# Performance work log

Hardware: AMD Instinct MI355X
Metric: run time of the kernel (lower is better)

The kernel has to match this reference:

```python
import jax, jax.numpy as jnp
import numpy as np

B, N, C = 4, 4096, 128

def setup_inputs() -> dict:
    key = jax.random.key(0)
    ks = jax.random.split(key, 7)
    s = 1.0 / np.sqrt(C)
    return {
        "x": jax.random.normal(ks[0], (B, N, C), dtype=jnp.float32),
        "Wq": jax.random.uniform(ks[1], (C, C), jnp.float32, -s, s),
        "bq": jax.random.uniform(ks[2], (C,), jnp.float32, -s, s),
        "Wk": jax.random.uniform(ks[3], (C, C), jnp.float32, -s, s),
        "bk": jax.random.uniform(ks[4], (C,), jnp.float32, -s, s),
        "Wv": jax.random.uniform(ks[5], (C, C), jnp.float32, -s, s),
        "bv": jax.random.uniform(ks[6], (C,), jnp.float32, -s, s),
    }

def reference(x, Wq, bq, Wk, bk, Wv, bv):
    # GELU-activated Q/K/V projections (torch default GELU = exact erf form)
    q = jax.nn.gelu(jnp.einsum("bnc,dc->bnd", x, Wq) + bq, approximate=False)
    k = jax.nn.gelu(jnp.einsum("bnc,dc->bnd", x, Wk) + bk, approximate=False)
    v = jax.nn.gelu(jnp.einsum("bnc,dc->bnd", x, Wv) + bv, approximate=False)
    # Unscaled attention: softmax(Q K^T) V
    scores = jnp.einsum("bnd,bmd->bnm", q, k)  # [B, N, N]
    attn = jax.nn.softmax(scores, axis=-1)
    return jnp.einsum("bnm,bmd->bnd", attn, v)
```

## Files before the change

### kernel.cpp

```cpp
#include <hip/hip_runtime.h>
#include <hip/hip_bf16.h>
#include <math.h>

#define BATCH 4
#define SEQ   4096
#define CDIM  128
#define NROWS (BATCH * SEQ)
#define KVB   32
#define NTILE (SEQ / KVB)
#define KTILE_B 8192
#define VTILE_B 8192
#define STAGE_B (KTILE_B + VTILE_B)
#define LOG2E 1.4426950408889634f

typedef __attribute__((ext_vector_type(4))) float    f32x4;
typedef __attribute__((ext_vector_type(8))) _Float16 half8;
typedef __attribute__((ext_vector_type(4))) short    bf16x4;
typedef __attribute__((ext_vector_type(8))) short    bf16x8;

__device__ __forceinline__ float bf2f(short s) {
  unsigned u = ((unsigned)(unsigned short)s) << 16;
  return __builtin_bit_cast(float, u);
}
__device__ __forceinline__ short f2bf(float f) {
  __hip_bfloat16 h = __float2bfloat16(f);
  return __builtin_bit_cast(short, h);
}
__device__ __forceinline__ float gelu_exact(float v) {
  return 0.5f * v * (1.0f + erff(v * 0.70710678118654752440f));
}
__device__ __forceinline__ int kswz_h(int r, int c) {
  int slot  = c >> 3;
  int slotp = (slot & 8) | ((slot ^ r) & 7);
  return r * 128 + slotp * 8 + (c & 7);
}
__device__ __forceinline__ void gl_lds16(const void* g, void* l) {
  __builtin_amdgcn_global_load_lds(
      (const __attribute__((address_space(1))) void*)g,
      (__attribute__((address_space(3))) void*)l, 16, 0, 0);
}

__global__ void wprep_kernel(const float* __restrict__ Wq,
                             const float* __restrict__ Wk,
                             const float* __restrict__ Wv,
                             _Float16* __restrict__ wfrag) {
  int mat = blockIdx.y;
  const float* W = (mat == 0) ? Wq : ((mat == 1) ? Wk : Wv);
  int i = blockIdx.x * 256 + threadIdx.x;
  int d = i >> 7, c = i & 127;
  int nt = d >> 4, qr = d & 15, cc = c >> 5, g = (c >> 3) & 3, j = c & 7;
  wfrag[(size_t)((((mat * 8 + nt) * 4 + cc) * 64) + 16 * g + qr) * 8 + j] =
      (_Float16)W[i];
}

__global__ __launch_bounds__(256) void proj_kernel(
    const float* __restrict__ x, const _Float16* __restrict__ wfrag,
    const float* __restrict__ bq, const float* __restrict__ bk,
    const float* __restrict__ bv,
    _Float16* __restrict__ qfrag, _Float16* __restrict__ kimg,
    short* __restrict__ vimg) {
  __shared__ __align__(16) char pls[16384];
  const int tid = threadIdx.x, wave = tid >> 6, lane = tid & 63;
  const int g = lane >> 4, qr = lane & 15;
  const int row0 = blockIdx.x * 64 + wave * 16;

  half8 xf[4];
#pragma unroll
  for (int c4 = 0; c4 < 4; ++c4) {
    const float* px = x + (size_t)(row0 + qr) * CDIM + 8 * g + 32 * c4;
    f32x4 a = *(const f32x4*)px;
    f32x4 bb = *(const f32x4*)(px + 4);
    half8 hx;
#pragma unroll
    for (int j = 0; j < 4; ++j) { hx[j] = (_Float16)a[j]; hx[4 + j] = (_Float16)bb[j]; }
    xf[c4] = hx;
  }

#pragma unroll
  for (int mat = 0; mat < 3; ++mat) {
    const float* bias = (mat == 0) ? bq : ((mat == 1) ? bk : bv);
    f32x4 acc[8];
#pragma unroll
    for (int nt = 0; nt < 8; ++nt) acc[nt] = (f32x4){0.f, 0.f, 0.f, 0.f};
#pragma unroll
    for (int nt = 0; nt < 8; ++nt)
#pragma unroll
      for (int c4 = 0; c4 < 4; ++c4) {
        half8 wf = *(const half8*)(wfrag +
            ((size_t)(((mat * 8 + nt) * 4 + c4) * 64) + lane) * 8);
        acc[nt] = __builtin_amdgcn_mfma_f32_16x16x32_f16(xf[c4], wf, acc[nt], 0, 0, 0);
      }

    short* ls = (short*)pls;
#pragma unroll
    for (int nt = 0; nt < 8; ++nt) {
      int col = 16 * nt + qr;
      float bi = bias[col];
#pragma unroll
      for (int r = 0; r < 4; ++r) {
        int rl = wave * 16 + 4 * g + r;
        float val = gelu_exact(acc[nt][r] + bi);
        int off;
        short sv;
        if (mat == 0) {
          int lane2 = ((col >> 3) & 3) * 16 + (rl & 15);
          off = ((wave * 4 + (col >> 5)) * 64 + lane2) * 8 + (col & 7);
          sv = __builtin_bit_cast(short, (_Float16)(val * LOG2E));
        } else if (mat == 1) {
          int tl = rl >> 5, rr = rl & 31;
          off = tl * 4096 + kswz_h(rr, col);
          sv = __builtin_bit_cast(short, (_Float16)val);
        } else {
          int tl = rl >> 5, rr = rl & 31;
          off = tl * 4096 + ((rr >> 2) * 128 + col) * 4 + (rr & 3);
          sv = f2bf(val);
        }
        ls[off] = sv;
      }
    }
    __syncthreads();
    char* gdst = (mat == 0) ? (char*)qfrag + (size_t)blockIdx.x * 16384
               : (mat == 1) ? (char*)kimg + (size_t)blockIdx.x * 16384
                            : (char*)vimg + (size_t)blockIdx.x * 16384;
#pragma unroll
    for (int p = 0; p < 4; ++p)
      ((f32x4*)gdst)[tid + 256 * p] = ((const f32x4*)pls)[tid + 256 * p];
    __syncthreads();
  }
}

__global__ __launch_bounds__(256, 2) void attn_kernel(
    const _Float16* __restrict__ qfrag, const char* __restrict__ kimg,
    const char* __restrict__ vimg, short* __restrict__ pacc,
    float* __restrict__ pml) {
  __shared__ __align__(16) char smem[2][STAGE_B];
  const int tid = threadIdx.x, wave = tid >> 6, lane = tid & 63;
  const int g = lane >> 4, qr = lane & 15;

  const int i = blockIdx.x;
  const int stream = i & 15;
  const int b = stream >> 2, quarter = stream & 3;
  const int qg = i >> 4;

  const int t0 = b * 256 + qg * 8 + wave * 2;
  half8 qf[2][4];
#pragma unroll
  for (int qs = 0; qs < 2; ++qs)
#pragma unroll
    for (int c4 = 0; c4 < 4; ++c4)
      qf[qs][c4] = *(const half8*)(qfrag +
          ((size_t)((t0 + qs) * 4 + c4) * 64 + lane) * 8);

  const char* kb_g = kimg + ((size_t)b * NTILE + quarter * 32) * KTILE_B;
  const char* vb_g = vimg + ((size_t)b * NTILE + quarter * 32) * VTILE_B;

  auto stage = [&](int t, char* buf) {
    const char* ks = kb_g + (size_t)t * KTILE_B;
    const char* vs = vb_g + (size_t)t * VTILE_B;
    gl_lds16(ks + tid * 16, buf + tid * 16);
    gl_lds16(ks + 4096 + tid * 16, buf + 4096 + tid * 16);
    gl_lds16(vs + tid * 16, buf + 8192 + tid * 16);
    gl_lds16(vs + 4096 + tid * 16, buf + 12288 + tid * 16);
  };

  f32x4 acc[2][8];
#pragma unroll
  for (int qs = 0; qs < 2; ++qs)
#pragma unroll
    for (int dt = 0; dt < 8; ++dt) acc[qs][dt] = (f32x4){0.f, 0.f, 0.f, 0.f};
  float m[2] = {-INFINITY, -INFINITY}, lsum[2] = {0.f, 0.f};

  stage(0, smem[0]);

  auto phase = [&](int t, char* cur, char* other, bool do_stage) {
    asm volatile("s_waitcnt vmcnt(0) lgkmcnt(0)" ::: "memory");
    __builtin_amdgcn_s_barrier();
    if (do_stage) stage(t + 1, other);

    f32x4 sA[2][2];
#pragma unroll
    for (int s = 0; s < 2; ++s) {
      half8 kf[4];
#pragma unroll
      for (int c4 = 0; c4 < 4; ++c4) {
        int slot = 4 * c4 + g;
        int slotp = (slot & 8) | ((slot ^ qr) & 7);
        kf[c4] = *(const half8*)(cur + (16 * s + qr) * 256 + slotp * 16);
      }
      __builtin_amdgcn_s_setprio(1);
#pragma unroll
      for (int qs = 0; qs < 2; ++qs) {
        f32x4 tac = (f32x4){0.f, 0.f, 0.f, 0.f};
#pragma unroll
        for (int c4 = 0; c4 < 4; ++c4)
          tac = __builtin_amdgcn_mfma_f32_16x16x32_f16(kf[c4], qf[qs][c4], tac, 0, 0, 0);
        sA[qs][s] = tac;
      }
      __builtin_amdgcn_s_setprio(0);
    }

    bf16x4 pf[2][2];
#pragma unroll
    for (int qs = 0; qs < 2; ++qs) {
      float tm = fmaxf(
          fmaxf(fmaxf(sA[qs][0][0], sA[qs][0][1]), fmaxf(sA[qs][0][2], sA[qs][0][3])),
          fmaxf(fmaxf(sA[qs][1][0], sA[qs][1][1]), fmaxf(sA[qs][1][2], sA[qs][1][3])));
      tm = fmaxf(tm, __shfl_xor(tm, 16, 64));
      tm = fmaxf(tm, __shfl_xor(tm, 32, 64));
      if (!__all(tm <= m[qs] + 8.0f)) {
        float mn = fmaxf(m[qs], tm);
        float alpha = exp2f(m[qs] - mn);
        m[qs] = mn;
        lsum[qs] *= alpha;
        float af[4];
#pragma unroll
        for (int r = 0; r < 4; ++r) af[r] = __shfl(alpha, 4 * g + r, 64);
#pragma unroll
        for (int dt = 0; dt < 8; ++dt)
#pragma unroll
          for (int r = 0; r < 4; ++r) acc[qs][dt][r] *= af[r];
      }
      float p[8], ps = 0.f;
#pragma unroll
      for (int e = 0; e < 8; ++e) {
        p[e] = exp2f(sA[qs][e >> 2][e & 3] - m[qs]);
        ps += p[e];
      }
      ps += __shfl_xor(ps, 16, 64);
      ps += __shfl_xor(ps, 32, 64);
      lsum[qs] += ps;
#pragma unroll
      for (int r = 0; r < 4; ++r) { pf[qs][0][r] = f2bf(p[r]); pf[qs][1][r] = f2bf(p[4 + r]); }
    }

    const char* vb = cur + KTILE_B;
#pragma unroll
    for (int dt = 0; dt < 8; ++dt) {
      bf16x4 v0 = *(const bf16x4*)(vb + g * 1024 + dt * 128 + qr * 8);
      bf16x4 v1 = *(const bf16x4*)(vb + 4096 + g * 1024 + dt * 128 + qr * 8);
      __builtin_amdgcn_s_setprio(1);
#pragma unroll
      for (int qs = 0; qs < 2; ++qs) {
        acc[qs][dt] = __builtin_amdgcn_mfma_f32_16x16x16bf16_1k(pf[qs][0], v0, acc[qs][dt], 0, 0, 0);
        acc[qs][dt] = __builtin_amdgcn_mfma_f32_16x16x16bf16_1k(pf[qs][1], v1, acc[qs][dt], 0, 0, 0);
      }
      __builtin_amdgcn_s_setprio(0);
    }
  };

  for (int it = 0; it < 16; ++it) {
    phase(2 * it,     smem[0], smem[1], true);
    phase(2 * it + 1, smem[1], smem[0], 2 * it + 2 < 32);
  }

  const int lrow0 = qg * 128 + wave * 32;
#pragma unroll
  for (int qs = 0; qs < 2; ++qs) {
#pragma unroll
    for (int dt = 0; dt < 8; ++dt)
#pragma unroll
      for (int r = 0; r < 4; ++r) {
        int grow = b * SEQ + lrow0 + qs * 16 + 4 * g + r;
        pacc[((size_t)quarter * NROWS + grow) * CDIM + 16 * dt + qr] =
            f2bf(acc[qs][dt][r]);
      }
    if (g == 0) {
      int grow = b * SEQ + lrow0 + qs * 16 + qr;
      pml[((size_t)quarter * NROWS + grow) * 2 + 0] = m[qs];
      pml[((size_t)quarter * NROWS + grow) * 2 + 1] = lsum[qs];
    }
  }
}

__global__ __launch_bounds__(256) void combine_kernel(
    const short* __restrict__ pacc, const float* __restrict__ pml,
    float* __restrict__ out) {
  int idx = blockIdx.x * 256 + threadIdx.x;
  int row = idx >> 4, c8 = idx & 15;
  float mm[4], ll[4];
  float M = -INFINITY;
#pragma unroll
  for (int h = 0; h < 4; ++h) {
    mm[h] = pml[((size_t)h * NROWS + row) * 2 + 0];
    ll[h] = pml[((size_t)h * NROWS + row) * 2 + 1];
    M = fmaxf(M, mm[h]);
  }
  float o[8];
#pragma unroll
  for (int j = 0; j < 8; ++j) o[j] = 0.f;
  float wl = 0.f;
#pragma unroll
  for (int h = 0; h < 4; ++h) {
    float w = exp2f(mm[h] - M);
    wl += w * ll[h];
    bf16x8 a = ((const bf16x8*)pacc)[((size_t)h * NROWS + row) * 16 + c8];
#pragma unroll
    for (int j = 0; j < 8; ++j) o[j] += w * bf2f(a[j]);
  }
  float inv = 1.0f / wl;
  f32x4 o0 = {o[0] * inv, o[1] * inv, o[2] * inv, o[3] * inv};
  f32x4 o1 = {o[4] * inv, o[5] * inv, o[6] * inv, o[7] * inv};
  ((f32x4*)out)[(size_t)row * 32 + c8 * 2 + 0] = o0;
  ((f32x4*)out)[(size_t)row * 32 + c8 * 2 + 1] = o1;
}

extern "C" void kernel_launch(void* const* d_in, const int* in_sizes, int n_in,
                              void* d_out, int out_size, void* d_ws, size_t ws_size,
                              hipStream_t stream) {
  const float* x  = (const float*)d_in[0];
  const float* Wq = (const float*)d_in[1];
  const float* bq = (const float*)d_in[2];
  const float* Wk = (const float*)d_in[3];
  const float* bk = (const float*)d_in[4];
  const float* Wv = (const float*)d_in[5];
  const float* bv = (const float*)d_in[6];
  float* out = (float*)d_out;

  char* ws = (char*)d_ws;
  _Float16* qfrag = (_Float16*)(ws);
  char*     kimg  = ws + (4u << 20);
  char*     vimg  = ws + (8u << 20);
  _Float16* wfrag = (_Float16*)(ws + (12u << 20));
  short*    pacc  = (short*)(ws + (12u << 20) + (256u << 10));
  float*    pml   = (float*)(ws + (28u << 20) + (512u << 10));

  wprep_kernel<<<dim3(64, 3), 256, 0, stream>>>(Wq, Wk, Wv, wfrag);
  proj_kernel<<<NROWS / 64, 256, 0, stream>>>(x, wfrag, bq, bk, bv,
                                              qfrag, (_Float16*)kimg, (short*)vimg);
  attn_kernel<<<512, 256, 0, stream>>>(qfrag, kimg, vimg, pacc, pml);
  combine_kernel<<<NROWS * 16 / 256, 256, 0, stream>>>(pacc, pml, out);
}
```

Before: 162.6 us.

## Split attention KV into eight chunks, raise occupancy, use hardware exp2

When the workspace is large enough, the KV sequence is split into eight chunks instead of four. This doubles the attention grid to 1024 blocks, and launch bounds now request 4 blocks per CU for more occupancy. It also precomputes the LDS swizzle offsets, advances the K/V pointers incrementally, and replaces exp2f with a raw v_exp_f32 instruction. In exchange, combine_kernel has twice the partial results to read and merge, there is more partial-output traffic, and the register cap may cause spills.

```diff
diff --git a/kernel.cpp b/kernel.cpp
--- a/kernel.cpp
+++ b/kernel.cpp
@@ -28,6 +28,11 @@
 }
 __device__ __forceinline__ float gelu_exact(float v) {
   return 0.5f * v * (1.0f + erff(v * 0.70710678118654752440f));
+}
+__device__ __forceinline__ float exp2_hw(float x) {
+  float r;
+  asm("v_exp_f32 %0, %1\n\ts_nop 0" : "=v"(r) : "v"(x));
+  return r;
 }
 __device__ __forceinline__ int kswz_h(int r, int c) {
   int slot  = c >> 3;
@@ -129,18 +134,20 @@
   }
 }
 
-__global__ __launch_bounds__(256, 2) void attn_kernel(
+template <int NSPLIT>
+__global__ __launch_bounds__(256, 4) void attn_kernel(
     const _Float16* __restrict__ qfrag, const char* __restrict__ kimg,
     const char* __restrict__ vimg, short* __restrict__ pacc,
     float* __restrict__ pml) {
   __shared__ __align__(16) char smem[2][STAGE_B];
+  constexpr int NT = NTILE / NSPLIT;
   const int tid = threadIdx.x, wave = tid >> 6, lane = tid & 63;
   const int g = lane >> 4, qr = lane & 15;
 
   const int i = blockIdx.x;
-  const int stream = i & 15;
-  const int b = stream >> 2, quarter = stream & 3;
-  const int qg = i >> 4;
+  const int stream = i & (4 * NSPLIT - 1);
+  const int b = stream / NSPLIT, sp = stream % NSPLIT;
+  const int qg = i / (4 * NSPLIT);
 
   const int t0 = b * 256 + qg * 8 + wave * 2;
   half8 qf[2][4];
@@ -151,16 +158,27 @@
       qf[qs][c4] = *(const half8*)(qfrag +
           ((size_t)((t0 + qs) * 4 + c4) * 64 + lane) * 8);
 
-  const char* kb_g = kimg + ((size_t)b * NTILE + quarter * 32) * KTILE_B;
-  const char* vb_g = vimg + ((size_t)b * NTILE + quarter * 32) * VTILE_B;
-
-  auto stage = [&](int t, char* buf) {
-    const char* ks = kb_g + (size_t)t * KTILE_B;
-    const char* vs = vb_g + (size_t)t * VTILE_B;
-    gl_lds16(ks + tid * 16, buf + tid * 16);
-    gl_lds16(ks + 4096 + tid * 16, buf + 4096 + tid * 16);
-    gl_lds16(vs + tid * 16, buf + 8192 + tid * 16);
-    gl_lds16(vs + 4096 + tid * 16, buf + 12288 + tid * 16);
+  int koff[8];
+#pragma unroll
+  for (int s = 0; s < 2; ++s)
+#pragma unroll
+    for (int c4 = 0; c4 < 4; ++c4) {
+      int slot = 4 * c4 + g;
+      int slotp = (slot & 8) | ((slot ^ qr) & 7);
+      koff[s * 4 + c4] = (16 * s + qr) * 256 + slotp * 16;
+    }
+  const int voff = g * 1024 + qr * 8;
+
+  const char* kp = kimg + ((size_t)b * NTILE + sp * NT) * KTILE_B + tid * 16;
+  const char* vp = vimg + ((size_t)b * NTILE + sp * NT) * VTILE_B + tid * 16;
+
+  auto stage = [&](char* buf) {
+    gl_lds16(kp,        buf + tid * 16);
+    gl_lds16(kp + 4096, buf + 4096 + tid * 16);
+    gl_lds16(vp,        buf + 8192 + tid * 16);
+    gl_lds16(vp + 4096, buf + 12288 + tid * 16);
+    kp += KTILE_B;
+    vp += VTILE_B;
   };
 
   f32x4 acc[2][8];
@@ -170,23 +188,20 @@
     for (int dt = 0; dt < 8; ++dt) acc[qs][dt] = (f32x4){0.f, 0.f, 0.f, 0.f};
   float m[2] = {-INFINITY, -INFINITY}, lsum[2] = {0.f, 0.f};
 
-  stage(0, smem[0]);
-
-  auto phase = [&](int t, char* cur, char* other, bool do_stage) {
+  stage(smem[0]);
+
+  auto phase = [&](const char* cur, char* other, bool do_stage) {
     asm volatile("s_waitcnt vmcnt(0) lgkmcnt(0)" ::: "memory");
     __builtin_amdgcn_s_barrier();
-    if (do_stage) stage(t + 1, other);
+    if (do_stage) stage(other);
 
     f32x4 sA[2][2];
 #pragma unroll
     for (int s = 0; s < 2; ++s) {
       half8 kf[4];
 #pragma unroll
-      for (int c4 = 0; c4 < 4; ++c4) {
-        int slot = 4 * c4 + g;
-        int slotp = (slot & 8) | ((slot ^ qr) & 7);
-        kf[c4] = *(const half8*)(cur + (16 * s + qr) * 256 + slotp * 16);
-      }
+      for (int c4 = 0; c4 < 4; ++c4)
+        kf[c4] = *(const half8*)(cur + koff[s * 4 + c4]);
       __builtin_amdgcn_s_setprio(1);
 #pragma unroll
       for (int qs = 0; qs < 2; ++qs) {
@@ -209,7 +224,7 @@
       tm = fmaxf(tm, __shfl_xor(tm, 32, 64));
       if (!__all(tm <= m[qs] + 8.0f)) {
         float mn = fmaxf(m[qs], tm);
-        float alpha = exp2f(m[qs] - mn);
+        float alpha = exp2_hw(m[qs] - mn);
         m[qs] = mn;
         lsum[qs] *= alpha;
         float af[4];
@@ -223,7 +238,7 @@
       float p[8], ps = 0.f;
 #pragma unroll
       for (int e = 0; e < 8; ++e) {
-        p[e] = exp2f(sA[qs][e >> 2][e & 3] - m[qs]);
+        p[e] = exp2_hw(sA[qs][e >> 2][e & 3] - m[qs]);
         ps += p[e];
       }
       ps += __shfl_xor(ps, 16, 64);
@@ -233,11 +248,11 @@
       for (int r = 0; r < 4; ++r) { pf[qs][0][r] = f2bf(p[r]); pf[qs][1][r] = f2bf(p[4 + r]); }
     }
 
-    const char* vb = cur + KTILE_B;
+    const char* vb = cur + KTILE_B + voff;
 #pragma unroll
     for (int dt = 0; dt < 8; ++dt) {
-      bf16x4 v0 = *(const bf16x4*)(vb + g * 1024 + dt * 128 + qr * 8);
-      bf16x4 v1 = *(const bf16x4*)(vb + 4096 + g * 1024 + dt * 128 + qr * 8);
+      bf16x4 v0 = *(const bf16x4*)(vb + dt * 128);
+      bf16x4 v1 = *(const bf16x4*)(vb + 4096 + dt * 128);
       __builtin_amdgcn_s_setprio(1);
 #pragma unroll
       for (int qs = 0; qs < 2; ++qs) {
@@ -248,9 +263,10 @@
     }
   };
 
-  for (int it = 0; it < 16; ++it) {
-    phase(2 * it,     smem[0], smem[1], true);
-    phase(2 * it + 1, smem[1], smem[0], 2 * it + 2 < 32);
+#pragma unroll 1
+  for (int it = 0; it < NT / 2; ++it) {
+    phase(smem[0], smem[1], true);
+    phase(smem[1], smem[0], it != NT / 2 - 1);
   }
 
   const int lrow0 = qg * 128 + wave * 32;
@@ -261,26 +277,27 @@
 #pragma unroll
       for (int r = 0; r < 4; ++r) {
         int grow = b * SEQ + lrow0 + qs * 16 + 4 * g + r;
-        pacc[((size_t)quarter * NROWS + grow) * CDIM + 16 * dt + qr] =
+        pacc[((size_t)sp * NROWS + grow) * CDIM + 16 * dt + qr] =
             f2bf(acc[qs][dt][r]);
       }
     if (g == 0) {
       int grow = b * SEQ + lrow0 + qs * 16 + qr;
-      pml[((size_t)quarter * NROWS + grow) * 2 + 0] = m[qs];
-      pml[((size_t)quarter * NROWS + grow) * 2 + 1] = lsum[qs];
-    }
-  }
-}
-
+      pml[((size_t)sp * NROWS + grow) * 2 + 0] = m[qs];
+      pml[((size_t)sp * NROWS + grow) * 2 + 1] = lsum[qs];
+    }
+  }
+}
+
+template <int NSPLIT>
 __global__ __launch_bounds__(256) void combine_kernel(
     const short* __restrict__ pacc, const float* __restrict__ pml,
     float* __restrict__ out) {
   int idx = blockIdx.x * 256 + threadIdx.x;
   int row = idx >> 4, c8 = idx & 15;
-  float mm[4], ll[4];
+  float mm[NSPLIT], ll[NSPLIT];
   float M = -INFINITY;
 #pragma unroll
-  for (int h = 0; h < 4; ++h) {
+  for (int h = 0; h < NSPLIT; ++h) {
     mm[h] = pml[((size_t)h * NROWS + row) * 2 + 0];
     ll[h] = pml[((size_t)h * NROWS + row) * 2 + 1];
     M = fmaxf(M, mm[h]);
@@ -290,7 +307,7 @@
   for (int j = 0; j < 8; ++j) o[j] = 0.f;
   float wl = 0.f;
 #pragma unroll
-  for (int h = 0; h < 4; ++h) {
+  for (int h = 0; h < NSPLIT; ++h) {
     float w = exp2f(mm[h] - M);
     wl += w * ll[h];
     bf16x8 a = ((const bf16x8*)pacc)[((size_t)h * NROWS + row) * 16 + c8];
@@ -321,12 +338,23 @@
   char*     kimg  = ws + (4u << 20);
   char*     vimg  = ws + (8u << 20);
   _Float16* wfrag = (_Float16*)(ws + (12u << 20));
-  short*    pacc  = (short*)(ws + (12u << 20) + (256u << 10));
-  float*    pml   = (float*)(ws + (28u << 20) + (512u << 10));
+  char*     tail  = ws + (12u << 20) + (256u << 10);
+
+  const size_t need8 = (12u << 20) + (256u << 10) +
+                       (size_t)8 * NROWS * 8 + (size_t)8 * NROWS * CDIM * 2;
 
   wprep_kernel<<<dim3(64, 3), 256, 0, stream>>>(Wq, Wk, Wv, wfrag);
   proj_kernel<<<NROWS / 64, 256, 0, stream>>>(x, wfrag, bq, bk, bv,
                                               qfrag, (_Float16*)kimg, (short*)vimg);
-  attn_kernel<<<512, 256, 0, stream>>>(qfrag, kimg, vimg, pacc, pml);
-  combine_kernel<<<NROWS * 16 / 256, 256, 0, stream>>>(pacc, pml, out);
-}
+  if (ws_size >= need8) {
+    float* pml  = (float*)tail;
+    short* pacc = (short*)(tail + (size_t)8 * NROWS * 8);
+    attn_kernel<8><<<1024, 256, 0, stream>>>(qfrag, kimg, vimg, pacc, pml);
+    combine_kernel<8><<<NROWS * 16 / 256, 256, 0, stream>>>(pacc, pml, out);
+  } else {
+    float* pml  = (float*)tail;
+    short* pacc = (short*)(tail + (size_t)4 * NROWS * 8);
+    attn_kernel<4><<<512, 256, 0, stream>>>(qfrag, kimg, vimg, pacc, pml);
+    combine_kernel<4><<<NROWS * 16 / 256, 256, 0, stream>>>(pacc, pml, out);
+  }
+}
```

Measured after the change: 267.4 us. 64.5% more time.
